# Kernel tuning notes

Measured on AMD Instinct MI355X. Metric: run time of the kernel, lower is better.

## Reference

```python
import jax, jax.numpy as jnp
import numpy as np

B, H, C, PX, PY = 2, 16, 4, 16, 16
EXTRA = 64
HD = 64
N = C * PX * PY + EXTRA


def setup_inputs() -> dict:
    key = jax.random.key(0)
    ks = jax.random.split(key, 8)
    q = jax.random.normal(ks[0], (B, H, N, HD), jnp.float32)
    k = jax.random.normal(ks[1], (B, H, N, HD), jnp.float32)
    v = jax.random.normal(ks[2], (B, H, N, HD), jnp.float32)
    # valid SE(3) world-to-camera matrices: rotation via QR (det fixed to +1)
    A = jax.random.normal(ks[3], (B, C, 3, 3), jnp.float32)
    Q, _ = jnp.linalg.qr(A)
    det = jnp.linalg.det(Q)
    Q = Q * det[..., None, None]
    t = 0.5 * jax.random.normal(ks[4], (B, C, 3), jnp.float32)
    top = jnp.concatenate([Q, t[..., None]], -1)
    bot = jnp.broadcast_to(jnp.array([0.0, 0.0, 0.0, 1.0], jnp.float32), (B, C, 1, 4))
    viewmats = jnp.concatenate([top, bot], -2)
    # pinhole intrinsics (no skew)
    fx = 300.0 + 10.0 * jax.random.uniform(ks[5], (B, C))
    fy = 300.0 + 10.0 * jax.random.uniform(ks[6], (B, C))
    z = jnp.zeros((B, C)); o = jnp.ones((B, C))
    cx = 128.0 * o; cy = 128.0 * o
    Ks = jnp.stack([jnp.stack([fx, z, cx], -1), jnp.stack([z, fy, cy], -1), jnp.stack([z, z, o], -1)], -2)
    spatial_mask = jnp.arange(N) >= EXTRA  # first EXTRA tokens are non-spatial
    return {"q": q, "k": k, "v": v, "viewmats": viewmats, "Ks": Ks,
            "spatial_mask": spatial_mask, "patches_x": PX, "patches_y": PY,
            "image_width": 256, "image_height": 256}


def _invert_SE3(T):
    R = T[..., :3, :3]; t = T[..., :3, 3]
    Rinv = jnp.swapaxes(R, -1, -2)
    tinv = -jnp.einsum('...ij,...j->...i', Rinv, t)
    top = jnp.concatenate([Rinv, tinv[..., None]], -1)
    bot = jnp.broadcast_to(jnp.array([0.0, 0.0, 0.0, 1.0], T.dtype), T.shape[:-2] + (1, 4))
    return jnp.concatenate([top, bot], -2)


def _lift(K3):
    out = jnp.zeros(K3.shape[:-2] + (4, 4), K3.dtype)
    return out.at[..., :3, :3].set(K3).at[..., 3, 3].set(1.0)


def _invert_K(K):
    fx = K[..., 0, 0]; fy = K[..., 1, 1]; cx = K[..., 0, 2]; cy = K[..., 1, 2]
    z = jnp.zeros_like(fx); o = jnp.ones_like(fx)
    return jnp.stack([jnp.stack([1.0 / fx, z, -cx / fx], -1),
                      jnp.stack([z, 1.0 / fy, -cy / fy], -1),
                      jnp.stack([z, z, o], -1)], -2)


def _transform(feats, M, cosx, sinx, cosy, siny, inverse):
    # Block-diagonal: [tiled 4x4 projmat on D/2 | RoPE-x on D/4 | RoPE-y on D/4]
    Bq, Hq, Nq, D = feats.shape
    h2 = D // 2; h4 = D // 4
    p = feats[..., :h2].reshape(Bq, Hq, Nq, h2 // 4, 4)
    p = jnp.einsum('bnij,bhnkj->bhnki', M, p).reshape(Bq, Hq, Nq, h2)

    def rope(x, c, s):
        c = c[None, None]; s = s[None, None]  # [1,1,N,nf]
        xa, xb = x[..., : x.shape[-1] // 2], x[..., x.shape[-1] // 2:]
        if inverse:
            return jnp.concatenate([c * xa - s * xb, s * xa + c * xb], -1)
        return jnp.concatenate([c * xa + s * xb, -s * xa + c * xb], -1)

    rx = rope(feats[..., h2:h2 + h4], cosx, sinx)
    ry = rope(feats[..., h2 + h4:], cosy, siny)
    return jnp.concatenate([p, rx, ry], -1)


def reference(q, k, v, viewmats, Ks, spatial_mask, patches_x, patches_y, image_width, image_height):
    D = q.shape[-1]
    Bq, Cq = viewmats.shape[:2]
    # normalized intrinsics
    fx = Ks[..., 0, 0] / image_width; fy = Ks[..., 1, 1] / image_height
    cx = Ks[..., 0, 2] / image_width - 0.5; cy = Ks[..., 1, 2] / image_height - 0.5
    z = jnp.zeros_like(fx); o = jnp.ones_like(fx)
    Kn = jnp.stack([jnp.stack([fx, z, cx], -1), jnp.stack([z, fy, cy], -1), jnp.stack([z, z, o], -1)], -2)
    P = jnp.einsum('...ij,...jk->...ik', _lift(Kn), viewmats)          # [B,C,4,4]
    P_T = jnp.swapaxes(P, -1, -2)
    P_inv = jnp.einsum('...ij,...jk->...ik', _invert_SE3(viewmats), _lift(_invert_K(Kn)))
    # RoPE tables over spatial tokens (split convention, base=100, scale=1)
    nf = D // 8
    freqs = 100.0 ** (-jnp.arange(nf, dtype=jnp.float32) / nf)
    pos_x = jnp.tile(jnp.arange(patches_x, dtype=jnp.float32), patches_y * Cq)
    pos_y = jnp.tile(jnp.repeat(jnp.arange(patches_y, dtype=jnp.float32), patches_x), Cq)
    ang_x = pos_x[:, None] * freqs; ang_y = pos_y[:, None] * freqs  # [S,nf]
    mask = spatial_mask
    S = pos_x.shape[0]
    # index of each token within the spatial-token ordering (masked scatter, vectorized)
    sidx = jnp.clip(jnp.cumsum(mask.astype(jnp.int32)) - 1, 0, S - 1)
    m = mask[:, None]
    cosx = jnp.where(m, jnp.cos(ang_x)[sidx], 1.0); sinx = jnp.where(m, jnp.sin(ang_x)[sidx], 0.0)
    cosy = jnp.where(m, jnp.cos(ang_y)[sidx], 1.0); siny = jnp.where(m, jnp.sin(ang_y)[sidx], 0.0)
    cam = sidx // (patches_x * patches_y)  # camera id per token
    I4 = jnp.eye(4, dtype=q.dtype)
    mm = mask[None, :, None, None]
    Mq = jnp.where(mm, P_T[:, cam], I4)    # [B,N,4,4]
    Mkv = jnp.where(mm, P_inv[:, cam], I4)
    Mo = jnp.where(mm, P[:, cam], I4)
    qt = _transform(q, Mq, cosx, sinx, cosy, siny, False)
    kt = _transform(k, Mkv, cosx, sinx, cosy, siny, False)
    vt = _transform(v, Mkv, cosx, sinx, cosy, siny, False)
    logits = jnp.einsum('bhqd,bhkd->bhqk', qt, kt) / jnp.sqrt(jnp.float32(D))
    attn = jax.nn.softmax(logits, axis=-1)
    out = jnp.einsum('bhqk,bhkd->bhqd', attn, vt)
    return _transform(out, Mo, cosx, sinx, cosy, siny, True)
```

## Files before the change

kernel.cpp:

```cpp
#include <hip/hip_runtime.h>
#include <math.h>

typedef _Float16 f16;
typedef _Float16 f16x8 __attribute__((ext_vector_type(8)));
typedef __fp16 h16x2 __attribute__((ext_vector_type(2)));
typedef float f32x16 __attribute__((ext_vector_type(16)));
typedef unsigned int u32;
typedef u32 u32x4 __attribute__((ext_vector_type(4)));

constexpr int Bc = 2, Hc = 16, Cc = 4, PXc = 16, PYc = 16, EXTRAc = 64, HDc = 64;
constexpr int Nc = Cc * PXc * PYc + EXTRAc;
constexpr int BH = Bc * Hc;
constexpr int KT = 64;
constexpr int NKT = Nc / KT;
constexpr int KS = 4;
constexpr int NQT = Nc / 32;

constexpr size_t TENS_SZ  = (size_t)BH * Nc * HDc * 2;
constexpr size_t PBH      = (size_t)Nc * 128;
constexpr size_t QF_OFF   = 0;
constexpr size_t KF_OFF   = QF_OFF + TENS_SZ;
constexpr size_t VT_OFF   = KF_OFF + TENS_SZ;
constexpr size_t PART_OFF = VT_OFF + TENS_SZ;
constexpr size_t ML_OFF   = PART_OFF + (size_t)KS * TENS_SZ;

__device__ const float FREQS[8] = {1.0f, 0.5623413252f, 0.31622776601f, 0.17782794100f,
                                   0.1f, 0.05623413252f, 0.031622776602f, 0.017782794100f};
constexpr float QSCALE = 0.125f * 1.4426950408889634f;

__device__ __forceinline__ void compute_M(float* M, const float* __restrict__ vm,
                                          const float* __restrict__ Ks3, int b, int cam, int which) {
    const float* V  = vm + (b * Cc + cam) * 16;
    const float* K3 = Ks3 + (b * Cc + cam) * 9;
    float fx = K3[0] * (1.0f / 256.0f);
    float fy = K3[4] * (1.0f / 256.0f);
    float cx = K3[2] * (1.0f / 256.0f) - 0.5f;
    float cy = K3[5] * (1.0f / 256.0f) - 0.5f;
    if (which == 2) {
        float IV[16];
        IV[0] = V[0]; IV[1] = V[4]; IV[2] = V[8];
        IV[4] = V[1]; IV[5] = V[5]; IV[6] = V[9];
        IV[8] = V[2]; IV[9] = V[6]; IV[10] = V[10];
        float tx = V[3], ty = V[7], tz = V[11];
        IV[3]  = -(IV[0] * tx + IV[1] * ty + IV[2] * tz);
        IV[7]  = -(IV[4] * tx + IV[5] * ty + IV[6] * tz);
        IV[11] = -(IV[8] * tx + IV[9] * ty + IV[10] * tz);
        IV[12] = 0.f; IV[13] = 0.f; IV[14] = 0.f; IV[15] = 1.f;
        float ifx = 1.f / fx, ify = 1.f / fy;
        float ncx = -cx * ifx, ncy = -cy * ify;
        #pragma unroll
        for (int i = 0; i < 4; ++i) {
            M[i * 4 + 0] = IV[i * 4 + 0] * ifx;
            M[i * 4 + 1] = IV[i * 4 + 1] * ify;
            M[i * 4 + 2] = IV[i * 4 + 0] * ncx + IV[i * 4 + 1] * ncy + IV[i * 4 + 2];
            M[i * 4 + 3] = IV[i * 4 + 3];
        }
    } else {
        float P[16];
        #pragma unroll
        for (int j = 0; j < 4; ++j) {
            P[0 * 4 + j] = fx * V[0 * 4 + j] + cx * V[2 * 4 + j];
            P[1 * 4 + j] = fy * V[1 * 4 + j] + cy * V[2 * 4 + j];
            P[2 * 4 + j] = V[2 * 4 + j];
            P[3 * 4 + j] = V[3 * 4 + j];
        }
        if (which == 0) {
            #pragma unroll
            for (int i = 0; i < 16; ++i) M[i] = P[i];
        } else {
            #pragma unroll
            for (int i = 0; i < 4; ++i)
                #pragma unroll
                for (int j = 0; j < 4; ++j) M[i * 4 + j] = P[j * 4 + i];
        }
    }
}

template <bool INV>
__device__ __forceinline__ void xf_seg(float* v16, int seg, int n, int b, int which,
                                       const float* __restrict__ vm, const float* __restrict__ Ks3) {
    if (n < EXTRAc) return;
    int sidx = n - EXTRAc;
    int cam = sidx >> 8;
    if (seg < 2) {
        float M[16];
        compute_M(M, vm, Ks3, b, cam, which);
        #pragma unroll
        for (int g = 0; g < 4; ++g) {
            float a0 = v16[4 * g], a1 = v16[4 * g + 1], a2 = v16[4 * g + 2], a3 = v16[4 * g + 3];
            v16[4 * g + 0] = M[0]  * a0 + M[1]  * a1 + M[2]  * a2 + M[3]  * a3;
            v16[4 * g + 1] = M[4]  * a0 + M[5]  * a1 + M[6]  * a2 + M[7]  * a3;
            v16[4 * g + 2] = M[8]  * a0 + M[9]  * a1 + M[10] * a2 + M[11] * a3;
            v16[4 * g + 3] = M[12] * a0 + M[13] * a1 + M[14] * a2 + M[15] * a3;
        }
    } else {
        float pos = (seg == 2) ? (float)(sidx & (PXc - 1)) : (float)((sidx >> 4) & (PYc - 1));
        #pragma unroll
        for (int f = 0; f < 8; ++f) {
            float s, c;
            __sincosf(pos * FREQS[f], &s, &c);
            float xa = v16[f], xb = v16[8 + f];
            if (INV) {
                v16[f]     = c * xa - s * xb;
                v16[8 + f] = s * xa + c * xb;
            } else {
                v16[f]     = c * xa + s * xb;
                v16[8 + f] = -s * xa + c * xb;
            }
        }
    }
}

__device__ __forceinline__ u32 pkh(float a, float b) {
    h16x2 r = __builtin_amdgcn_cvt_pkrtz(a, b);
    return __builtin_bit_cast(u32, r);
}

__device__ __forceinline__ f32x16 zero16() {
    f32x16 z = {0.f,0.f,0.f,0.f,0.f,0.f,0.f,0.f,0.f,0.f,0.f,0.f,0.f,0.f,0.f,0.f};
    return z;
}

__global__ void prope_xform_kernel(const float* __restrict__ q, const float* __restrict__ k,
                                   const float* __restrict__ v,
                                   const float* __restrict__ viewmats, const float* __restrict__ Ks,
                                   char* __restrict__ wsb) {
    __shared__ f16 tile[64][72];
    if (blockIdx.x < 1088) {
        int id = blockIdx.x * 256 + threadIdx.x;
        int seg = id & 3;
        int rid = id >> 2;
        int tensor = rid / (BH * Nc);
        int row = rid - tensor * (BH * Nc);
        int n = row % Nc;
        int bhq = row / Nc;
        int b = bhq >> 4;
        const float* src = (tensor ? k : q) + (size_t)row * 64 + seg * 16;
        float vals[16];
        #pragma unroll
        for (int i = 0; i < 4; ++i) ((float4*)vals)[i] = ((const float4*)src)[i];
        xf_seg<false>(vals, seg, n, b, tensor ? 2 : 1, viewmats, Ks);
        float scale = tensor ? 1.0f : QSCALE;
        f16 o[16];
        #pragma unroll
        for (int i = 0; i < 16; ++i) o[i] = (f16)(vals[i] * scale);
        if (tensor == 0) {
            char* base = wsb + QF_OFF + (size_t)bhq * PBH + (size_t)(n >> 5) * 4096;
            int qq = n & 31;
            *(float4*)(base + (seg * 2 + 0) * 512 + qq * 16) = ((float4*)o)[0];
            *(float4*)(base + (seg * 2 + 1) * 512 + qq * 16) = ((float4*)o)[1];
        } else {
            char* base = wsb + KF_OFF + (size_t)bhq * PBH + (size_t)(n >> 6) * 8192;
            int kk = n & 63, rh = kk >> 5, qq = kk & 31;
            *(float4*)(base + (((seg * 2 + rh) * 2 + 0) * 32 + qq) * 16) = ((float4*)o)[0];
            *(float4*)(base + (((seg * 2 + rh) * 2 + 1) * 32 + qq) * 16) = ((float4*)o)[1];
        }
    } else {
        int vb = blockIdx.x - 1088;
        int kt = vb >> 5, bh = vb & 31;
        int b = bh >> 4;
        int t = threadIdx.x;
        {
            int r = t >> 2, seg = t & 3;
            int n = kt * 64 + r;
            const float* src = v + ((size_t)bh * Nc + n) * 64 + seg * 16;
            float vals[16];
            #pragma unroll
            for (int i = 0; i < 4; ++i) ((float4*)vals)[i] = ((const float4*)src)[i];
            xf_seg<false>(vals, seg, n, b, 2, viewmats, Ks);
            #pragma unroll
            for (int i = 0; i < 16; ++i) tile[r][seg * 16 + i] = (f16)vals[i];
        }
        __syncthreads();
        {
            int d = t >> 2, ks = t & 3;
            f16 o[16];
            #pragma unroll
            for (int j = 0; j < 16; ++j) o[j] = tile[ks * 16 + j][d];
            int dh = d >> 5, dq = d & 31;
            char* base = wsb + VT_OFF + (size_t)bh * PBH + (size_t)kt * 8192;
            *(float4*)(base + (((ks * 2 + dh) * 2 + 0) * 32 + dq) * 16) = ((float4*)o)[0];
            *(float4*)(base + (((ks * 2 + dh) * 2 + 1) * 32 + dq) * 16) = ((float4*)o)[1];
        }
    }
}

__global__ __launch_bounds__(64, 3) void prope_attn_mfma_kernel(
    const char* __restrict__ wsb, char* __restrict__ partO, float* __restrict__ partML) {
    __shared__ char ob[4096];

    const int lane = threadIdx.x;
    const int q = lane & 31, h = lane >> 5;
    const int qt = blockIdx.x, bh = blockIdx.y, z = blockIdx.z;
    const int ts = (NKT * z) / KS, te = (NKT * (z + 1)) / KS;

    const char* kfb = wsb + KF_OFF + (size_t)bh * PBH;
    const char* vfb = wsb + VT_OFF + (size_t)bh * PBH;
    const char* qfb = wsb + QF_OFF + (size_t)bh * PBH + (size_t)qt * 4096;

    f16x8 qb[4];
    #pragma unroll
    for (int c = 0; c < 4; ++c) qb[c] = *(const f16x8*)(qfb + c * 1024 + lane * 16);

    f32x16 o0 = zero16(), o1 = zero16();
    float mrun = -1e30f, lrun = 0.f;

    for (int it = ts; it < te; ++it) {
        const char* kb = kfb + (size_t)it * 8192;
        const char* vb = vfb + (size_t)it * 8192;

        f16x8 ka0[4], ka1[4];
        #pragma unroll
        for (int c = 0; c < 4; ++c) {
            ka0[c] = *(const f16x8*)(kb + (c * 2 + 0) * 1024 + lane * 16);
            ka1[c] = *(const f16x8*)(kb + (c * 2 + 1) * 1024 + lane * 16);
        }

        f32x16 s0 = zero16(), s1 = zero16();
        #pragma unroll
        for (int c = 0; c < 4; ++c) {
            s0 = __builtin_amdgcn_mfma_f32_32x32x16_f16(ka0[c], qb[c], s0, 0, 0, 0);
            s1 = __builtin_amdgcn_mfma_f32_32x32x16_f16(ka1[c], qb[c], s1, 0, 0, 0);
        }

        f16x8 va0[4], va1[4];
        #pragma unroll
        for (int c = 0; c < 4; ++c) {
            va0[c] = *(const f16x8*)(vb + (c * 2 + 0) * 1024 + lane * 16);
            va1[c] = *(const f16x8*)(vb + (c * 2 + 1) * 1024 + lane * 16);
        }

        float tm = -1e30f;
        #pragma unroll
        for (int i = 0; i < 16; ++i) { tm = fmaxf(tm, s0[i]); tm = fmaxf(tm, s1[i]); }
        tm = fmaxf(tm, __shfl_xor(tm, 32, 64));
        float nm = fmaxf(mrun, tm);
        float corr = exp2f(mrun - nm);
        mrun = nm;
        float p0[16], p1[16];
        float ps = 0.f;
        #pragma unroll
        for (int i = 0; i < 16; ++i) { p0[i] = exp2f(s0[i] - nm); ps += p0[i]; }
        #pragma unroll
        for (int i = 0; i < 16; ++i) { p1[i] = exp2f(s1[i] - nm); ps += p1[i]; }
        ps += __shfl_xor(ps, 32, 64);
        lrun = lrun * corr + ps;
        #pragma unroll
        for (int i = 0; i < 16; ++i) { o0[i] *= corr; o1[i] *= corr; }

        u32 U0[8], U1[8];
        #pragma unroll
        for (int g = 0; g < 4; ++g) {
            U0[g * 2 + 0] = pkh(p0[4 * g + 0], p0[4 * g + 1]);
            U0[g * 2 + 1] = pkh(p0[4 * g + 2], p0[4 * g + 3]);
            U1[g * 2 + 0] = pkh(p1[4 * g + 0], p1[4 * g + 1]);
            U1[g * 2 + 1] = pkh(p1[4 * g + 2], p1[4 * g + 3]);
        }

        #pragma unroll
        for (int c = 0; c < 4; ++c) {
            const u32* Us = (c < 2) ? U0 : U1;
            int gl = 2 * (c & 1);
            u32 x0 = Us[(gl + 1) * 2 + 0], x1 = Us[(gl + 1) * 2 + 1];
            u32 y0 = Us[gl * 2 + 0],       y1 = Us[gl * 2 + 1];
            u32 s0w = h ? y0 : x0;
            u32 s1w = h ? y1 : x1;
            u32 r0 = (u32)__shfl_xor((int)s0w, 32, 64);
            u32 r1 = (u32)__shfl_xor((int)s1w, 32, 64);
            u32 own0 = h ? x0 : y0, own1 = h ? x1 : y1;
            u32 w0 = h ? r0 : own0;
            u32 w1 = h ? r1 : own1;
            u32 w2 = h ? own0 : r0;
            u32 w3 = h ? own1 : r1;
            u32x4 fw = {w0, w1, w2, w3};
            f16x8 pb = __builtin_bit_cast(f16x8, fw);
            o0 = __builtin_amdgcn_mfma_f32_32x32x16_f16(va0[c], pb, o0, 0, 0, 0);
            o1 = __builtin_amdgcn_mfma_f32_32x32x16_f16(va1[c], pb, o1, 0, 0, 0);
        }
    }

    float invl = 1.f / lrun;
    #pragma unroll
    for (int g = 0; g < 4; ++g) {
        #pragma unroll
        for (int w = 0; w < 2; ++w) {
            u32 u0 = pkh(o0[4 * g + 2 * w] * invl, o0[4 * g + 2 * w + 1] * invl);
            u32 u1 = pkh(o1[4 * g + 2 * w] * invl, o1[4 * g + 2 * w + 1] * invl);
            int col0 = 16 * g + 8 * h + 4 * w;
            *(u32*)(ob + ((q * 128 + col0) ^ ((q & 7) << 4))) = u0;
            *(u32*)(ob + ((q * 128 + col0 + 64) ^ ((q & 7) << 4))) = u1;
        }
    }
    if (h == 0) {
        float2 mlv = {mrun, lrun};
        ((float2*)partML)[((size_t)z * BH + bh) * Nc + qt * 32 + q] = mlv;
    }
    __syncthreads();
    {
        int r = lane >> 1, half = lane & 1;
        char* dst = partO + (((size_t)z * BH + bh) * Nc + qt * 32 + r) * 128 + half * 64;
        #pragma unroll
        for (int j = 0; j < 4; ++j) {
            float4 val = *(float4*)(ob + ((r * 128 + half * 64 + j * 16) ^ ((r & 7) << 4)));
            ((float4*)dst)[j] = val;
        }
    }
}

__global__ void prope_combine_kernel(const char* __restrict__ wsb,
                                     const float* __restrict__ viewmats, const float* __restrict__ Ks,
                                     float* __restrict__ out) {
    int id = blockIdx.x * 256 + threadIdx.x;
    int seg = id & 3, rid = id >> 2;
    int n = rid % Nc, bh = rid / Nc, b = bh >> 4;
    const float2* ml = (const float2*)(wsb + ML_OFF);
    float m[KS], l[KS];
    float mstar = -1e30f;
    #pragma unroll
    for (int s = 0; s < KS; ++s) {
        float2 v = ml[((size_t)s * BH + bh) * Nc + n];
        m[s] = v.x; l[s] = v.y;
        mstar = fmaxf(mstar, m[s]);
    }
    float wsum = 0.f, wgt[KS];
    #pragma unroll
    for (int s = 0; s < KS; ++s) { wgt[s] = exp2f(m[s] - mstar) * l[s]; wsum += wgt[s]; }
    float inv = 1.f / wsum;
    float acc[16];
    #pragma unroll
    for (int i = 0; i < 16; ++i) acc[i] = 0.f;
    #pragma unroll
    for (int s = 0; s < KS; ++s) {
        const char* op = wsb + PART_OFF + (((size_t)s * BH + bh) * Nc + n) * 128 + seg * 32;
        f16x8 a0 = *(const f16x8*)op;
        f16x8 a1 = *(const f16x8*)(op + 16);
        #pragma unroll
        for (int i = 0; i < 8; ++i) acc[i] += wgt[s] * (float)a0[i];
        #pragma unroll
        for (int i = 0; i < 8; ++i) acc[8 + i] += wgt[s] * (float)a1[i];
    }
    #pragma unroll
    for (int i = 0; i < 16; ++i) acc[i] *= inv;
    xf_seg<true>(acc, seg, n, b, 0, viewmats, Ks);
    float* go = out + ((size_t)bh * Nc + n) * 64 + seg * 16;
    #pragma unroll
    for (int i = 0; i < 4; ++i) ((float4*)go)[i] = ((const float4*)acc)[i];
}

extern "C" void kernel_launch(void* const* d_in, const int* in_sizes, int n_in,
                              void* d_out, int out_size, void* d_ws, size_t ws_size,
                              hipStream_t stream) {
    const float* q        = (const float*)d_in[0];
    const float* k        = (const float*)d_in[1];
    const float* v        = (const float*)d_in[2];
    const float* viewmats = (const float*)d_in[3];
    const float* Ks       = (const float*)d_in[4];
    char* wsb  = (char*)d_ws;
    float* out = (float*)d_out;

    prope_xform_kernel<<<1088 + 544, 256, 0, stream>>>(q, k, v, viewmats, Ks, wsb);
    prope_attn_mfma_kernel<<<dim3(NQT, BH, KS), 64, 0, stream>>>(wsb, wsb + PART_OFF,
                                                                 (float*)(wsb + ML_OFF));
    prope_combine_kernel<<<(BH * Nc * 4) / 256, 256, 0, stream>>>(wsb, viewmats, Ks, out);
}
```

Before: 48.03 us.

## Double-buffer K tiles, add lazy softmax rescale and XCD-aware block remap

Restructures the attention loop so the next K tile is prefetched into registers while the current tile's QK MFMAs and softmax run, ping-ponging between two register buffers. It also skips the running-max rescale unless the new max exceeds the old one by more than a threshold, uses tree reductions for max and sum, and raises MFMA priority with s_setprio. The grid becomes 1D with an XCD-interleaving remap so neighbouring tiles of the same head share an L2. Launch bounds drop from 3 to 2 waves per SIMD to make room for the extra registers, which may lower occupancy.

```diff
diff --git a/kernel.cpp b/kernel.cpp
--- a/kernel.cpp
+++ b/kernel.cpp
@@ -15,6 +15,7 @@
 constexpr int NKT = Nc / KT;
 constexpr int KS = 4;
 constexpr int NQT = Nc / 32;
+constexpr int NBLK = NQT * BH * KS;
 
 constexpr size_t TENS_SZ  = (size_t)BH * Nc * HDc * 2;
 constexpr size_t PBH      = (size_t)Nc * 128;
@@ -185,13 +186,112 @@
     }
 }
 
-__global__ __launch_bounds__(64, 3) void prope_attn_mfma_kernel(
+struct KF { f16x8 a0[4]; f16x8 a1[4]; };
+
+__device__ __forceinline__ void load_kf(KF& kf, const char* kb, int lane) {
+    #pragma unroll
+    for (int c = 0; c < 4; ++c) {
+        kf.a0[c] = *(const f16x8*)(kb + (c * 2 + 0) * 1024 + lane * 16);
+        kf.a1[c] = *(const f16x8*)(kb + (c * 2 + 1) * 1024 + lane * 16);
+    }
+}
+
+__device__ __forceinline__ void tile_step(
+    const KF& kc, KF& kn, bool pre, const char* vb, const char* kbn,
+    const f16x8 (&qb)[4], int lane, int h,
+    f32x16& o0, f32x16& o1, float& mrun, float& lrun)
+{
+    f32x16 s0 = zero16(), s1 = zero16();
+    __builtin_amdgcn_s_setprio(1);
+    #pragma unroll
+    for (int c = 0; c < 4; ++c) {
+        s0 = __builtin_amdgcn_mfma_f32_32x32x16_f16(kc.a0[c], qb[c], s0, 0, 0, 0);
+        s1 = __builtin_amdgcn_mfma_f32_32x32x16_f16(kc.a1[c], qb[c], s1, 0, 0, 0);
+    }
+    __builtin_amdgcn_s_setprio(0);
+    if (pre) load_kf(kn, kbn, lane);
+    f16x8 va0[4], va1[4];
+    #pragma unroll
+    for (int c = 0; c < 4; ++c) {
+        va0[c] = *(const f16x8*)(vb + (c * 2 + 0) * 1024 + lane * 16);
+        va1[c] = *(const f16x8*)(vb + (c * 2 + 1) * 1024 + lane * 16);
+    }
+
+    float q8[8];
+    #pragma unroll
+    for (int i = 0; i < 4; ++i) {
+        q8[i]     = fmaxf(fmaxf(s0[4*i], s0[4*i+1]), fmaxf(s0[4*i+2], s0[4*i+3]));
+        q8[4 + i] = fmaxf(fmaxf(s1[4*i], s1[4*i+1]), fmaxf(s1[4*i+2], s1[4*i+3]));
+    }
+    float tm = fmaxf(fmaxf(fmaxf(q8[0], q8[1]), fmaxf(q8[2], q8[3])),
+                     fmaxf(fmaxf(q8[4], q8[5]), fmaxf(q8[6], q8[7])));
+    tm = fmaxf(tm, __shfl_xor(tm, 32, 64));
+    if (!__all(tm <= mrun + 8.0f)) {
+        float nm = fmaxf(mrun, tm);
+        float corr = exp2f(mrun - nm);
+        mrun = nm;
+        lrun *= corr;
+        #pragma unroll
+        for (int i = 0; i < 16; ++i) { o0[i] *= corr; o1[i] *= corr; }
+    }
+    #pragma unroll
+    for (int i = 0; i < 16; ++i) s0[i] = exp2f(s0[i] - mrun);
+    #pragma unroll
+    for (int i = 0; i < 16; ++i) s1[i] = exp2f(s1[i] - mrun);
+    float a8[8];
+    #pragma unroll
+    for (int i = 0; i < 4; ++i) {
+        a8[i]     = (s0[4*i] + s0[4*i+1]) + (s0[4*i+2] + s0[4*i+3]);
+        a8[4 + i] = (s1[4*i] + s1[4*i+1]) + (s1[4*i+2] + s1[4*i+3]);
+    }
+    float ps = ((a8[0] + a8[1]) + (a8[2] + a8[3])) + ((a8[4] + a8[5]) + (a8[6] + a8[7]));
+    ps += __shfl_xor(ps, 32, 64);
+    lrun += ps;
+
+    u32 U0[8], U1[8];
+    #pragma unroll
+    for (int g = 0; g < 4; ++g) {
+        U0[g * 2 + 0] = pkh(s0[4 * g + 0], s0[4 * g + 1]);
+        U0[g * 2 + 1] = pkh(s0[4 * g + 2], s0[4 * g + 3]);
+        U1[g * 2 + 0] = pkh(s1[4 * g + 0], s1[4 * g + 1]);
+        U1[g * 2 + 1] = pkh(s1[4 * g + 2], s1[4 * g + 3]);
+    }
+
+    #pragma unroll
+    for (int c = 0; c < 4; ++c) {
+        const u32* Us = (c < 2) ? U0 : U1;
+        int gl = 2 * (c & 1);
+        u32 x0 = Us[(gl + 1) * 2 + 0], x1 = Us[(gl + 1) * 2 + 1];
+        u32 y0 = Us[gl * 2 + 0],       y1 = Us[gl * 2 + 1];
+        u32 s0w = h ? y0 : x0;
+        u32 s1w = h ? y1 : x1;
+        u32 r0 = (u32)__shfl_xor((int)s0w, 32, 64);
+        u32 r1 = (u32)__shfl_xor((int)s1w, 32, 64);
+        u32 own0 = h ? x0 : y0, own1 = h ? x1 : y1;
+        u32 w0 = h ? r0 : own0;
+        u32 w1 = h ? r1 : own1;
+        u32 w2 = h ? own0 : r0;
+        u32 w3 = h ? own1 : r1;
+        u32x4 fw = {w0, w1, w2, w3};
+        f16x8 pb = __builtin_bit_cast(f16x8, fw);
+        __builtin_amdgcn_s_setprio(1);
+        o0 = __builtin_amdgcn_mfma_f32_32x32x16_f16(va0[c], pb, o0, 0, 0, 0);
+        o1 = __builtin_amdgcn_mfma_f32_32x32x16_f16(va1[c], pb, o1, 0, 0, 0);
+        __builtin_amdgcn_s_setprio(0);
+    }
+}
+
+__global__ __launch_bounds__(64, 2) void prope_attn_mfma_kernel(
     const char* __restrict__ wsb, char* __restrict__ partO, float* __restrict__ partML) {
     __shared__ char ob[4096];
 
     const int lane = threadIdx.x;
     const int q = lane & 31, h = lane >> 5;
-    const int qt = blockIdx.x, bh = blockIdx.y, z = blockIdx.z;
+    const int bid = blockIdx.x;
+    const int l = (bid & 7) * (NBLK / 8) + (bid >> 3);
+    const int qt = l % NQT;
+    const int r  = l / NQT;
+    const int bh = r & 31, z = r >> 5;
     const int ts = (NKT * z) / KS, te = (NKT * (z + 1)) / KS;
 
     const char* kfb = wsb + KF_OFF + (size_t)bh * PBH;
@@ -205,78 +305,16 @@
     f32x16 o0 = zero16(), o1 = zero16();
     float mrun = -1e30f, lrun = 0.f;
 
-    for (int it = ts; it < te; ++it) {
-        const char* kb = kfb + (size_t)it * 8192;
-        const char* vb = vfb + (size_t)it * 8192;
-
-        f16x8 ka0[4], ka1[4];
-        #pragma unroll
-        for (int c = 0; c < 4; ++c) {
-            ka0[c] = *(const f16x8*)(kb + (c * 2 + 0) * 1024 + lane * 16);
-            ka1[c] = *(const f16x8*)(kb + (c * 2 + 1) * 1024 + lane * 16);
-        }
-
-        f32x16 s0 = zero16(), s1 = zero16();
-        #pragma unroll
-        for (int c = 0; c < 4; ++c) {
-            s0 = __builtin_amdgcn_mfma_f32_32x32x16_f16(ka0[c], qb[c], s0, 0, 0, 0);
-            s1 = __builtin_amdgcn_mfma_f32_32x32x16_f16(ka1[c], qb[c], s1, 0, 0, 0);
-        }
-
-        f16x8 va0[4], va1[4];
-        #pragma unroll
-        for (int c = 0; c < 4; ++c) {
-            va0[c] = *(const f16x8*)(vb + (c * 2 + 0) * 1024 + lane * 16);
-            va1[c] = *(const f16x8*)(vb + (c * 2 + 1) * 1024 + lane * 16);
-        }
-
-        float tm = -1e30f;
-        #pragma unroll
-        for (int i = 0; i < 16; ++i) { tm = fmaxf(tm, s0[i]); tm = fmaxf(tm, s1[i]); }
-        tm = fmaxf(tm, __shfl_xor(tm, 32, 64));
-        float nm = fmaxf(mrun, tm);
-        float corr = exp2f(mrun - nm);
-        mrun = nm;
-        float p0[16], p1[16];
-        float ps = 0.f;
-        #pragma unroll
-        for (int i = 0; i < 16; ++i) { p0[i] = exp2f(s0[i] - nm); ps += p0[i]; }
-        #pragma unroll
-        for (int i = 0; i < 16; ++i) { p1[i] = exp2f(s1[i] - nm); ps += p1[i]; }
-        ps += __shfl_xor(ps, 32, 64);
-        lrun = lrun * corr + ps;
-        #pragma unroll
-        for (int i = 0; i < 16; ++i) { o0[i] *= corr; o1[i] *= corr; }
-
-        u32 U0[8], U1[8];
-        #pragma unroll
-        for (int g = 0; g < 4; ++g) {
-            U0[g * 2 + 0] = pkh(p0[4 * g + 0], p0[4 * g + 1]);
-            U0[g * 2 + 1] = pkh(p0[4 * g + 2], p0[4 * g + 3]);
-            U1[g * 2 + 0] = pkh(p1[4 * g + 0], p1[4 * g + 1]);
-            U1[g * 2 + 1] = pkh(p1[4 * g + 2], p1[4 * g + 3]);
-        }
-
-        #pragma unroll
-        for (int c = 0; c < 4; ++c) {
-            const u32* Us = (c < 2) ? U0 : U1;
-            int gl = 2 * (c & 1);
-            u32 x0 = Us[(gl + 1) * 2 + 0], x1 = Us[(gl + 1) * 2 + 1];
-            u32 y0 = Us[gl * 2 + 0],       y1 = Us[gl * 2 + 1];
-            u32 s0w = h ? y0 : x0;
-            u32 s1w = h ? y1 : x1;
-            u32 r0 = (u32)__shfl_xor((int)s0w, 32, 64);
-            u32 r1 = (u32)__shfl_xor((int)s1w, 32, 64);
-            u32 own0 = h ? x0 : y0, own1 = h ? x1 : y1;
-            u32 w0 = h ? r0 : own0;
-            u32 w1 = h ? r1 : own1;
-            u32 w2 = h ? own0 : r0;
-            u32 w3 = h ? own1 : r1;
-            u32x4 fw = {w0, w1, w2, w3};
-            f16x8 pb = __builtin_bit_cast(f16x8, fw);
-            o0 = __builtin_amdgcn_mfma_f32_32x32x16_f16(va0[c], pb, o0, 0, 0, 0);
-            o1 = __builtin_amdgcn_mfma_f32_32x32x16_f16(va1[c], pb, o1, 0, 0, 0);
-        }
+    KF kA, kB;
+    load_kf(kA, kfb + (size_t)ts * 8192, lane);
+    int it = ts;
+    for (;;) {
+        tile_step(kA, kB, it + 1 < te, vfb + (size_t)it * 8192,
+                  kfb + (size_t)(it + 1) * 8192, qb, lane, h, o0, o1, mrun, lrun);
+        if (++it >= te) break;
+        tile_step(kB, kA, it + 1 < te, vfb + (size_t)it * 8192,
+                  kfb + (size_t)(it + 1) * 8192, qb, lane, h, o0, o1, mrun, lrun);
+        if (++it >= te) break;
     }
 
     float invl = 1.f / lrun;
@@ -297,11 +335,11 @@
     }
     __syncthreads();
     {
-        int r = lane >> 1, half = lane & 1;
-        char* dst = partO + (((size_t)z * BH + bh) * Nc + qt * 32 + r) * 128 + half * 64;
+        int rr = lane >> 1, half = lane & 1;
+        char* dst = partO + (((size_t)z * BH + bh) * Nc + qt * 32 + rr) * 128 + half * 64;
         #pragma unroll
         for (int j = 0; j < 4; ++j) {
-            float4 val = *(float4*)(ob + ((r * 128 + half * 64 + j * 16) ^ ((r & 7) << 4)));
+            float4 val = *(float4*)(ob + ((rr * 128 + half * 64 + j * 16) ^ ((rr & 7) << 4)));
             ((float4*)dst)[j] = val;
         }
     }
@@ -359,7 +397,7 @@
     float* out = (float*)d_out;
 
     prope_xform_kernel<<<1088 + 544, 256, 0, stream>>>(q, k, v, viewmats, Ks, wsb);
-    prope_attn_mfma_kernel<<<dim3(NQT, BH, KS), 64, 0, stream>>>(wsb, wsb + PART_OFF,
-                                                                 (float*)(wsb + ML_OFF));
+    prope_attn_mfma_kernel<<<NBLK, 64, 0, stream>>>(wsb, wsb + PART_OFF,
+                                                    (float*)(wsb + ML_OFF));
     prope_combine_kernel<<<(BH * Nc * 4) / 256, 256, 0, stream>>>(wsb, viewmats, Ks, out);
 }
```

Result: slower. 50.64 us (+5.4%).
